# Kernel optimization log

Measured on AMD Instinct MI355X. Metric: run time of the kernel, lower is better.

The kernel has to match this reference:

```python
import jax, jax.numpy as jnp
import numpy as np

ALPHA = 0.25
GAMMA = 2.0
EPS = 1e-8


def _pairwise_giou_loss(pred, true):
    # pred: (b,1,N,4), true: (b,m,1,4); boxes in [y1,x1,y2,x2] (tfa convention)
    py1, px1, py2, px2 = [pred[..., i] for i in range(4)]
    ty1, tx1, ty2, tx2 = [true[..., i] for i in range(4)]
    p_area = jnp.maximum(py2 - py1, 0.0) * jnp.maximum(px2 - px1, 0.0)
    t_area = jnp.maximum(ty2 - ty1, 0.0) * jnp.maximum(tx2 - tx1, 0.0)
    i_h = jnp.maximum(jnp.minimum(py2, ty2) - jnp.maximum(py1, ty1), 0.0)
    i_w = jnp.maximum(jnp.minimum(px2, tx2) - jnp.maximum(px1, tx1), 0.0)
    inter = i_h * i_w
    union = p_area + t_area - inter
    iou = jnp.where(union > 0, inter / jnp.maximum(union, EPS), 0.0)
    e_h = jnp.maximum(py2, ty2) - jnp.minimum(py1, ty1)
    e_w = jnp.maximum(px2, tx2) - jnp.minimum(px1, tx1)
    enclose = e_h * e_w
    giou = iou - jnp.where(enclose > 0, (enclose - union) / jnp.maximum(enclose, EPS), 0.0)
    return 1.0 - giou  # (b,m,N)


def setup_inputs():
    key = jax.random.key(0)
    k1, k2, k3, k4 = jax.random.split(key, 4)
    b, w, h, c, m = 8, 128, 128, 80, 100
    # probabilities in (0,1) as produced by a sigmoid head
    cls_pred = jax.random.uniform(k1, (b, w, h, c), jnp.float32, 1e-4, 1.0 - 1e-4)
    # raw box coords in grid units (divided by [w,h,w,h] inside the module)
    loc_pred = jax.random.uniform(k2, (b, w, h, 4), jnp.float32) * jnp.asarray([w, h, w, h], jnp.float32)
    labels = jax.random.randint(k3, (b, m), 0, c)
    cls_true = jax.nn.one_hot(labels, c, dtype=jnp.float32)
    loc_true = jax.random.uniform(k4, (b, m, 4), jnp.float32)
    reg_mask = jnp.ones((b, m), jnp.float32)
    return {"cls_pred": cls_pred, "loc_pred": loc_pred, "cls_true": cls_true,
            "loc_true": loc_true, "reg_mask": reg_mask}


def reference(cls_pred, loc_pred, cls_true, loc_true, reg_mask):
    b, w, h, c = cls_pred.shape
    m = cls_true.shape[1]
    cls_true = (cls_true == 1).astype(jnp.float32)
    p = cls_pred.reshape(b, w * h, c)                                      # (b,N,c)
    loc_p = loc_pred.reshape(b, w * h, 4) / jnp.asarray([w, h, w, h], jnp.float32)
    # focal-style pos/neg class costs; contract over c instead of materializing (b,m,N,c)
    neg = (1.0 - ALPHA) * p ** GAMMA * (-jnp.log(1.0 - p + EPS))
    pos = ALPHA * (1.0 - p) ** GAMMA * (-jnp.log(p + EPS))
    cls_loss = jnp.einsum('bnc,bmc->bmn', pos - neg, cls_true)             # (b,m,N)
    reg_loss = jnp.sum(jnp.abs(loc_true[:, :, None, :] - loc_p[:, None, :, :]), axis=-1)
    giou_loss = _pairwise_giou_loss(loc_p[:, None, :, :], loc_true[:, :, None, :])
    total = 2.0 * cls_loss + 5.0 * reg_loss + 2.0 * giou_loss              # (b,m,N)
    argmin_total = jnp.argmin(total, axis=-1).astype(jnp.int32)            # (b,m)
    batch_idx = jnp.broadcast_to(jnp.arange(b, dtype=jnp.int32)[:, None], (b, m))
    cls_id = jnp.argmax(cls_true, axis=-1).astype(jnp.int32)
    return jnp.stack([batch_idx, argmin_total, cls_id], axis=-1)           # (b,m,3) int32
```

## Files before the change

kernel.cpp:

```cpp
#include <hip/hip_runtime.h>
#include <stdint.h>

#define B    8
#define C    80
#define M    100
#define NPIX 16384
#define NT   32
#define BT   128
#define NW   4

#define ALPHA_F 0.25f
#define EPS_F   1e-8f

#define SWZ(c) ((((c) & 31)) ^ ((((c) >> 5)) << 3))

__device__ __forceinline__ uint32_t fkey(float f) {
    uint32_t u = __float_as_uint(f);
    return (u & 0x80000000u) ? ~u : (u | 0x80000000u);
}

__global__ __launch_bounds__(256) void init_kernel(
    const float* __restrict__ cls_true,
    int* __restrict__ cids,
    unsigned long long* __restrict__ keys)
{
    const int bm   = blockIdx.x * NW + (threadIdx.x >> 6);
    const int lane = threadIdx.x & 63;
    if (bm >= B * M) return;

    const float* ct = cls_true + (size_t)bm * C;
    const float v0 = ct[lane];
    unsigned long long k =
        ((unsigned long long)fkey(v0) << 32) | (unsigned int)(C - 1 - lane);
    if (lane + 64 < C) {
        const float v1 = ct[lane + 64];
        unsigned long long k1 =
            ((unsigned long long)fkey(v1) << 32) | (unsigned int)(C - 1 - (lane + 64));
        if (k1 > k) k = k1;
    }
    #pragma unroll
    for (int off = 32; off > 0; off >>= 1) {
        unsigned long long o = __shfl_xor(k, off, 64);
        if (o > k) k = o;
    }
    if (lane == 0) {
        cids[bm] = C - 1 - (int)(k & 0xFFFFFFFFull);
        keys[bm] = 0xFFFFFFFFFFFFFFFFull;
    }
}

__global__ __launch_bounds__(BT, 6) void match_kernel(
    const float* __restrict__ cls_pred,
    const float* __restrict__ loc_pred,
    const float* __restrict__ loc_true,
    const int*   __restrict__ cids,
    unsigned long long* __restrict__ keys)
{
#pragma clang fp contract(off)
    __shared__ float  D[C * NT];
    __shared__ float4 bx4[NT];
    __shared__ float  bpa[NT];

    const int b    = blockIdx.y;
    const int n0   = blockIdx.x * NT;
    const int tid  = threadIdx.x;
    const int lane = tid & 63;
    const int w    = tid >> 6;

    const float4* src4 = (const float4*)(cls_pred + ((size_t)b * NPIX + n0) * C);
    #pragma unroll
    for (int it = 0; it < NT * C / 4 / BT; ++it) {
        const int idx4 = it * BT + tid;
        const int n    = idx4 / 20;
        const int c0   = (idx4 - n * 20) * 4;
        const float4 v = src4[idx4];
        const float pv[4] = { v.x, v.y, v.z, v.w };
        #pragma unroll
        for (int jj = 0; jj < 4; ++jj) {
            const int c = c0 + jj;
            const float p = pv[jj];
            const float q = 1.0f - p;
            const float pos = (ALPHA_F * (q * q)) * (-logf(p + EPS_F));
            const float neg = ((1.0f - ALPHA_F) * (p * p)) * (-logf(q + EPS_F));
            D[c * NT + ((n ^ SWZ(c)) & (NT - 1))] = pos - neg;
        }
    }

    if (tid < NT) {
        const float inv = 1.0f / 128.0f;
        const float4 lp = *(const float4*)(loc_pred + ((size_t)b * NPIX + n0 + tid) * 4);
        const float py1 = lp.x * inv;
        const float px1 = lp.y * inv;
        const float py2 = lp.z * inv;
        const float px2 = lp.w * inv;
        bx4[tid] = make_float4(py1, px1, py2, px2);
        bpa[tid] = fmaxf(py2 - py1, 0.0f) * fmaxf(px2 - px1, 0.0f);
    }

    __syncthreads();

    const int mm = w * 64 + lane;
    if (mm < M) {
        const int bm  = b * M + mm;
        const int cid = cids[bm];
        const float4 lt = *(const float4*)(loc_true + (size_t)bm * 4);
        const float ty1 = lt.x, tx1 = lt.y, ty2 = lt.z, tx2 = lt.w;
        const float t_area = fmaxf(ty2 - ty1, 0.0f) * fmaxf(tx2 - tx1, 0.0f);

        const int drow = cid * NT;
        const int sw   = SWZ(cid) & (NT - 1);

        float bestv = __builtin_huge_valf();
        int   bestn = 0;

        #pragma unroll 8
        for (int j = 0; j < NT; ++j) {
            const float  d  = D[drow + (j ^ sw)];
            const float4 bx = bx4[j];
            const float  pa = bpa[j];
            const float py1 = bx.x, px1 = bx.y, py2 = bx.z, px2 = bx.w;

            const float r = ((fabsf(ty1 - py1) + fabsf(tx1 - px1))
                             + fabsf(ty2 - py2)) + fabsf(tx2 - px2);

            const float ih = fmaxf(fminf(py2, ty2) - fmaxf(py1, ty1), 0.0f);
            const float iw = fmaxf(fminf(px2, tx2) - fmaxf(px1, tx1), 0.0f);
            const float inter = ih * iw;
            const float uni   = (pa + t_area) - inter;
            const float iou   = (uni > 0.0f) ? (inter / fmaxf(uni, EPS_F)) : 0.0f;
            const float eh = fmaxf(py2, ty2) - fminf(py1, ty1);
            const float ew = fmaxf(px2, tx2) - fminf(px1, tx1);
            const float enc = eh * ew;
            const float pen = (enc > 0.0f) ? ((enc - uni) / fmaxf(enc, EPS_F)) : 0.0f;
            const float gl  = 1.0f - (iou - pen);

            const float total = ((2.0f * d) + (5.0f * r)) + (2.0f * gl);

            if (total < bestv) { bestv = total; bestn = n0 + j; }
        }

        const unsigned long long key =
            ((unsigned long long)fkey(bestv) << 32) | (unsigned int)bestn;
        atomicMin(&keys[bm], key);
    }
}

__global__ void write_out_kernel(const unsigned long long* __restrict__ keys,
                                 const int* __restrict__ cids,
                                 int* __restrict__ out) {
    int i = blockIdx.x * blockDim.x + threadIdx.x;
    if (i >= B * M) return;
    out[i * 3 + 0] = i / M;
    out[i * 3 + 1] = (int)(keys[i] & 0xFFFFFFFFull);
    out[i * 3 + 2] = cids[i];
}

extern "C" void kernel_launch(void* const* d_in, const int* in_sizes, int n_in,
                              void* d_out, int out_size, void* d_ws, size_t ws_size,
                              hipStream_t stream) {
    const float* cls_pred = (const float*)d_in[0];
    const float* loc_pred = (const float*)d_in[1];
    const float* cls_true = (const float*)d_in[2];
    const float* loc_true = (const float*)d_in[3];
    int* out = (int*)d_out;

    unsigned long long* keys = (unsigned long long*)d_ws;
    int* cids = (int*)((char*)d_ws + (size_t)B * M * sizeof(unsigned long long));

    init_kernel<<<(B * M + NW - 1) / NW, 256, 0, stream>>>(cls_true, cids, keys);
    match_kernel<<<dim3(NPIX / NT, B), BT, 0, stream>>>(
        cls_pred, loc_pred, loc_true, cids, keys);
    write_out_kernel<<<(B * M + 255) / 256, 256, 0, stream>>>(keys, cids, out);
}
```

Baseline: 65.78 us.

## Double pixel tile, split waves across pixel halves, use unswizzled row-major LDS

Raises the per-block pixel tile from 32 to 64 with 256 threads. Each pair of waves covers the 100 targets and each pair takes half the pixels, so all four waves do matching work instead of two idling. The class-cost tile is now stored row-major with float4 writes instead of transposed with an XOR swizzle. Box data is packed into 8-float rows, and the target loads move ahead of the barrier. Reads of D by class index may now hit LDS bank conflicts, and the larger block may lower occupancy.

```diff
diff --git a/kernel.cpp b/kernel.cpp
--- a/kernel.cpp
+++ b/kernel.cpp
@@ -5,14 +5,12 @@
 #define C    80
 #define M    100
 #define NPIX 16384
-#define NT   32
-#define BT   128
+#define NT   64
+#define BT   256
 #define NW   4
 
 #define ALPHA_F 0.25f
 #define EPS_F   1e-8f
-
-#define SWZ(c) ((((c) & 31)) ^ ((((c) >> 5)) << 3))
 
 __device__ __forceinline__ uint32_t fkey(float f) {
     uint32_t u = __float_as_uint(f);
@@ -57,9 +55,8 @@
     unsigned long long* __restrict__ keys)
 {
 #pragma clang fp contract(off)
-    __shared__ float  D[C * NT];
-    __shared__ float4 bx4[NT];
-    __shared__ float  bpa[NT];
+    __shared__ float D[NT * C];
+    __shared__ float BX[NT * 8];
 
     const int b    = blockIdx.y;
     const int n0   = blockIdx.x * NT;
@@ -71,19 +68,18 @@
     #pragma unroll
     for (int it = 0; it < NT * C / 4 / BT; ++it) {
         const int idx4 = it * BT + tid;
-        const int n    = idx4 / 20;
-        const int c0   = (idx4 - n * 20) * 4;
         const float4 v = src4[idx4];
         const float pv[4] = { v.x, v.y, v.z, v.w };
+        float fo[4];
         #pragma unroll
         for (int jj = 0; jj < 4; ++jj) {
-            const int c = c0 + jj;
             const float p = pv[jj];
             const float q = 1.0f - p;
             const float pos = (ALPHA_F * (q * q)) * (-logf(p + EPS_F));
             const float neg = ((1.0f - ALPHA_F) * (p * p)) * (-logf(q + EPS_F));
-            D[c * NT + ((n ^ SWZ(c)) & (NT - 1))] = pos - neg;
+            fo[jj] = pos - neg;
         }
+        *(float4*)&D[idx4 * 4] = make_float4(fo[0], fo[1], fo[2], fo[3]);
     }
 
     if (tid < NT) {
@@ -93,52 +89,53 @@
         const float px1 = lp.y * inv;
         const float py2 = lp.z * inv;
         const float px2 = lp.w * inv;
-        bx4[tid] = make_float4(py1, px1, py2, px2);
-        bpa[tid] = fmaxf(py2 - py1, 0.0f) * fmaxf(px2 - px1, 0.0f);
+        *(float4*)&BX[tid * 8] = make_float4(py1, px1, py2, px2);
+        BX[tid * 8 + 4] = fmaxf(py2 - py1, 0.0f) * fmaxf(px2 - px1, 0.0f);
     }
+
+    const int  mm  = (w & 1) * 64 + lane;
+    const int  bm  = b * M + (mm < M ? mm : 0);
+    const int  cid = cids[bm];
+    const float4 lt = *(const float4*)(loc_true + (size_t)bm * 4);
+    const float ty1 = lt.x, tx1 = lt.y, ty2 = lt.z, tx2 = lt.w;
+    const float t_area = fmaxf(ty2 - ty1, 0.0f) * fmaxf(tx2 - tx1, 0.0f);
 
     __syncthreads();
 
-    const int mm = w * 64 + lane;
+    const int jb = (w >> 1) * (NT / 2);
+    const float* Dp = &D[jb * C + cid];
+    const float* Bp = &BX[jb * 8];
+
+    float bestv = __builtin_huge_valf();
+    int   bestn = 0;
+
+    #pragma unroll
+    for (int j = 0; j < NT / 2; ++j) {
+        const float  d  = Dp[j * C];
+        const float4 bx = *(const float4*)&Bp[j * 8];
+        const float  pa = Bp[j * 8 + 4];
+        const float py1 = bx.x, px1 = bx.y, py2 = bx.z, px2 = bx.w;
+
+        const float r = ((fabsf(ty1 - py1) + fabsf(tx1 - px1))
+                         + fabsf(ty2 - py2)) + fabsf(tx2 - px2);
+
+        const float ih = fmaxf(fminf(py2, ty2) - fmaxf(py1, ty1), 0.0f);
+        const float iw = fmaxf(fminf(px2, tx2) - fmaxf(px1, tx1), 0.0f);
+        const float inter = ih * iw;
+        const float uni   = (pa + t_area) - inter;
+        const float iou   = (uni > 0.0f) ? (inter / fmaxf(uni, EPS_F)) : 0.0f;
+        const float eh = fmaxf(py2, ty2) - fminf(py1, ty1);
+        const float ew = fmaxf(px2, tx2) - fminf(px1, tx1);
+        const float enc = eh * ew;
+        const float pen = (enc > 0.0f) ? ((enc - uni) / fmaxf(enc, EPS_F)) : 0.0f;
+        const float gl  = 1.0f - (iou - pen);
+
+        const float total = ((2.0f * d) + (5.0f * r)) + (2.0f * gl);
+
+        if (total < bestv) { bestv = total; bestn = n0 + jb + j; }
+    }
+
     if (mm < M) {
-        const int bm  = b * M + mm;
-        const int cid = cids[bm];
-        const float4 lt = *(const float4*)(loc_true + (size_t)bm * 4);
-        const float ty1 = lt.x, tx1 = lt.y, ty2 = lt.z, tx2 = lt.w;
-        const float t_area = fmaxf(ty2 - ty1, 0.0f) * fmaxf(tx2 - tx1, 0.0f);
-
-        const int drow = cid * NT;
-        const int sw   = SWZ(cid) & (NT - 1);
-
-        float bestv = __builtin_huge_valf();
-        int   bestn = 0;
-
-        #pragma unroll 8
-        for (int j = 0; j < NT; ++j) {
-            const float  d  = D[drow + (j ^ sw)];
-            const float4 bx = bx4[j];
-            const float  pa = bpa[j];
-            const float py1 = bx.x, px1 = bx.y, py2 = bx.z, px2 = bx.w;
-
-            const float r = ((fabsf(ty1 - py1) + fabsf(tx1 - px1))
-                             + fabsf(ty2 - py2)) + fabsf(tx2 - px2);
-
-            const float ih = fmaxf(fminf(py2, ty2) - fmaxf(py1, ty1), 0.0f);
-            const float iw = fmaxf(fminf(px2, tx2) - fmaxf(px1, tx1), 0.0f);
-            const float inter = ih * iw;
-            const float uni   = (pa + t_area) - inter;
-            const float iou   = (uni > 0.0f) ? (inter / fmaxf(uni, EPS_F)) : 0.0f;
-            const float eh = fmaxf(py2, ty2) - fminf(py1, ty1);
-            const float ew = fmaxf(px2, tx2) - fminf(px1, tx1);
-            const float enc = eh * ew;
-            const float pen = (enc > 0.0f) ? ((enc - uni) / fmaxf(enc, EPS_F)) : 0.0f;
-            const float gl  = 1.0f - (iou - pen);
-
-            const float total = ((2.0f * d) + (5.0f * r)) + (2.0f * gl);
-
-            if (total < bestv) { bestv = total; bestn = n0 + j; }
-        }
-
         const unsigned long long key =
             ((unsigned long long)fkey(bestv) << 32) | (unsigned int)bestn;
         atomicMin(&keys[bm], key);
```

Result: slower. 231.8 us (+252.4%).
